# Kernel optimization log

Measured on AMD Instinct MI355X. Metric: run time of the kernel, lower is better.

## Reference

```python
import jax, jax.numpy as jnp
import numpy as np

# Module hyperparameters (from init_kwargs)
INPUT_SIZE = 1024
OUTPUT_SIZE = 1024
ORDER = 3
GRID_RANGE = (-1.0, 1.0)
GRID_COUNT = 8
CENTER_COUNT = GRID_COUNT + ORDER + 1  # 12

_lo, _hi = GRID_RANGE
_end_center = _hi + (_hi - _lo) * (ORDER + 1) / (GRID_COUNT - 1)
CENTERS = jnp.asarray(np.linspace(_lo, _end_center, CENTER_COUNT), dtype=jnp.float32)
ZOOM = (_hi - _lo) / 2.0
PAN = (_hi + _lo) / 2.0


def setup_inputs() -> dict:
    key = jax.random.key(0)
    k1, k2 = jax.random.split(key)
    x = jax.random.normal(k1, (4096, INPUT_SIZE), dtype=jnp.float32)
    coef = jax.random.normal(k2, (OUTPUT_SIZE, INPUT_SIZE, GRID_COUNT), dtype=jnp.float32) * 0.1
    return {"x": x, "coef": coef}


def _spline_basis(x):
    # x: [B, I] -> basis: [B, I, GRID_COUNT] via Cox-de Boor recursion
    xt = jnp.tanh(x) * ZOOM + PAN
    c = CENTERS
    xe = xt[..., None]  # [B, I, 1]
    # order-0: indicator of [c[i], c[i+1]) for i = 0..CENTER_COUNT-2
    b = ((xe >= c[:-1]) & (xe < c[1:])).astype(xt.dtype)  # [B, I, CENTER_COUNT-1]
    for k in range(1, ORDER + 1):
        n = CENTER_COUNT - k - 1
        c0, ck = c[:n], c[k:k + n]
        c1, ck1 = c[1:n + 1], c[k + 1:k + 1 + n]
        left = (xe - c0) / (ck - c0)          # [B, I, n]
        right = (ck1 - xe) / (ck1 - c1)       # [B, I, n]
        b = left * b[..., :n] + right * b[..., 1:n + 1]
    return b  # [B, I, GRID_COUNT]


def reference(x, coef):
    spline = _spline_basis(x)                      # [B, I, G]
    # sum_j over inputs of coef-weighted basis: [B, O]
    return jnp.einsum('big,oig->bo', spline, coef)
```

## Files before the change

kernel.cpp:

```cpp
#include <hip/hip_runtime.h>
#include <stdint.h>
#include <stddef.h>


#define BATCH 4096
#define IN    1024
#define OUTN  1024
#define KDIM  (IN * 8)
#define NTT   (KDIM / 64)

typedef __attribute__((ext_vector_type(8)))  short          short8;
typedef __attribute__((ext_vector_type(8)))  unsigned short ushort8;
typedef __attribute__((ext_vector_type(4)))  float          f32x4;


__device__ __forceinline__ constexpr float Cf(int i) {
    constexpr double end  = 1.0 + 2.0 * 4.0 / 7.0;
    constexpr double step = (end - (-1.0)) / 11.0;
    return (float)(-1.0 + (double)i * step);
}

__device__ __forceinline__ unsigned short f2bf(float f) {
    unsigned int u = __builtin_bit_cast(unsigned int, f);
    u += 0x7fffu + ((u >> 16) & 1u);
    return (unsigned short)(u >> 16);
}

__device__ __forceinline__ float bf2f(unsigned short u) {
    unsigned int v = (unsigned int)u << 16;
    return __builtin_bit_cast(float, v);
}

__device__ __forceinline__ ushort8 spline8(float xt) {
    float v[11];
#pragma unroll
    for (int j = 0; j < 11; ++j)
        v[j] = (xt >= Cf(j) && xt < Cf(j + 1)) ? 1.0f : 0.0f;
#pragma unroll
    for (int k = 1; k <= 3; ++k) {
#pragma unroll
        for (int j = 0; j < 11 - k; ++j) {
            float left  = (xt - Cf(j))         * (1.0f / (Cf(j + k)     - Cf(j)));
            float right = (Cf(j + k + 1) - xt) * (1.0f / (Cf(j + k + 1) - Cf(j + 1)));
            v[j] = left * v[j] + right * v[j + 1];
        }
    }
    ushort8 r;
#pragma unroll
    for (int g = 0; g < 8; ++g) r[g] = f2bf(v[g]);
    return r;
}

typedef const unsigned int __attribute__((address_space(1))) gu32;
typedef unsigned int       __attribute__((address_space(3))) lu32;

__device__ __forceinline__ void gload_lds16(const void* g, void* l) {
    __builtin_amdgcn_global_load_lds((gu32*)g, (lu32*)l, 16, 0, 0);
}


__global__ void prep_kernel(const float* __restrict__ x, const float* __restrict__ coef,
                            unsigned short* __restrict__ A, unsigned short* __restrict__ B) {
    const int t = threadIdx.x;
    int blk = blockIdx.x;
    if (blk < 4096) {
        const int bb = blk >> 4, bi = blk & 15;
        const int b  = bb * 16 + (t & 15);
        const int i0 = bi * 64 + (t >> 4) * 4;
        f32x4 xv = *reinterpret_cast<const f32x4*>(&x[(size_t)b * IN + i0]);
        ushort8 r[4];
#pragma unroll
        for (int j = 0; j < 4; ++j) r[j] = spline8(tanhf(xv[j]));
        ushort8* out = reinterpret_cast<ushort8*>(A)
                     + ((size_t)(bb * 256 + bi * 16 + (t >> 4)) * 64) + (t & 15);
        out[0]  = r[0];
        out[16] = r[1];
        out[32] = r[2];
        out[48] = r[3];
    } else {
        blk -= 4096;
        const int ob = blk >> 4, ib = blk & 15;
        const int oo = ob * 16 + (t & 15);
        const int i0 = ib * 64 + (t >> 4) * 4;
        const f32x4* cin = reinterpret_cast<const f32x4*>(coef);
        ushort8 r[4];
#pragma unroll
        for (int j = 0; j < 4; ++j) {
            f32x4 v0 = cin[((size_t)oo * IN + i0 + j) * 2];
            f32x4 v1 = cin[((size_t)oo * IN + i0 + j) * 2 + 1];
#pragma unroll
            for (int g = 0; g < 4; ++g) { r[j][g] = f2bf(v0[g]); r[j][4 + g] = f2bf(v1[g]); }
        }
        ushort8* out = reinterpret_cast<ushort8*>(B)
                     + ((size_t)(ob * 256 + ib * 16 + (t >> 4)) * 64) + (t & 15);
        out[0]  = r[0];
        out[16] = r[1];
        out[32] = r[2];
        out[48] = r[3];
    }
}


#define LSA0 (&Ls[0][0])
#define LSB0 (&Ls[0][16384])
#define LSA1 (&Ls[1][0])
#define LSB1 (&Ls[1][16384])

template<int NSPLIT>
__global__ __launch_bounds__(512, 2) void gemm_bt(
        const unsigned short* __restrict__ Ashuf,
        const unsigned short* __restrict__ Bshuf,
        float* __restrict__ C,
        unsigned short* __restrict__ P) {
    constexpr int NT2 = NTT / NSPLIT;
    static_assert((NT2 & 1) == 0, "loop assumes even NT2");
    __shared__ unsigned short Ls[2][32768];

    const int tid  = threadIdx.x;
    const int w    = tid >> 6;
    const int lane = tid & 63;
    const int wm   = w >> 2, wn = w & 3;
    const int kkw  = w & 1, wh = w >> 1;
    const int lane8 = lane * 8;

    const int bid  = blockIdx.x;
    const int s    = bid & (NSPLIT - 1);
    const int tile = bid / NSPLIT;
    const int mb16 = (tile >> 2) * 16;
    const int nb16 = (tile & 3) * 16;
    const int T0   = s * NT2;
    const int brow = mb16 * 16, bcol = nb16 * 16;

#define STAGE_OP(BASE, NB16, H, T, LS) do {                                   \
        size_t _kq = ((size_t)(2 * (T0 + (T)) + kkw)) * 512 + lane8;          \
        const unsigned short* _g = (BASE) + ((size_t)((NB16) + (H)*8 + wh) << 17) + _kq; \
        unsigned short* _l = (LS) + (((H)*16 + w) << 9);                      \
        gload_lds16(_g, _l);                                                  \
        gload_lds16(_g + ((size_t)4 << 17), _l + (8 << 9));                   \
    } while (0)
#define STAGE_A(H, T, LS) STAGE_OP(Ashuf, mb16, H, T, LS)
#define STAGE_B(H, T, LS) STAGE_OP(Bshuf, nb16, H, T, LS)

#define LDA_F(DST, H, LS) do {                                                \
        _Pragma("unroll")                                                     \
        for (int mf = 0; mf < 4; ++mf)                                        \
            _Pragma("unroll")                                                 \
            for (int kk = 0; kk < 2; ++kk)                                    \
                DST[mf][kk] = *reinterpret_cast<const short8*>(               \
                    (LS) + (((((H)*8 + wm*4 + mf) * 2) + kk) << 9) + lane8);  \
    } while (0)
#define LDB_F(DST, V, LS) do {                                                \
        _Pragma("unroll")                                                     \
        for (int nf = 0; nf < 2; ++nf)                                        \
            _Pragma("unroll")                                                 \
            for (int kk = 0; kk < 2; ++kk)                                    \
                DST[nf][kk] = *reinterpret_cast<const short8*>(               \
                    (LS) + (((((V)*8 + wn*2 + nf) * 2) + kk) << 9) + lane8);  \
    } while (0)

    f32x4 acc[8][4] = {};
    short8 aF[4][2], bv0[2][2], bv1[2][2];

#define MFMA_Q(H, V, AF, BV) do {                                             \
        __builtin_amdgcn_s_setprio(1);                                        \
        _Pragma("unroll")                                                     \
        for (int kk = 0; kk < 2; ++kk)                                        \
            _Pragma("unroll")                                                 \
            for (int mf = 0; mf < 4; ++mf)                                    \
                _Pragma("unroll")                                             \
                for (int nf = 0; nf < 2; ++nf)                                \
                    acc[(H)*4 + mf][(V)*2 + nf] =                             \
                        __builtin_amdgcn_mfma_f32_16x16x32_bf16(              \
                            AF[mf][kk], BV[nf][kk],                           \
                            acc[(H)*4 + mf][(V)*2 + nf], 0, 0, 0);            \
        __builtin_amdgcn_s_setprio(0);                                        \
    } while (0)

#define TILE(T, LAC, LBC, LAN, LBN, S1F, S23F, RN, VC) do {                   \
        __builtin_amdgcn_s_barrier();                                         \
        MFMA_Q(0, 0, aF, bv0);                                                \
        LDB_F(bv1, 1, LBC);                                                   \
        if (S1F) { STAGE_B(1, (T) + 1, LBN); STAGE_A(1, (T) + 1, LAN); }      \
        __builtin_amdgcn_s_barrier();                                         \
        MFMA_Q(0, 1, aF, bv1);                                                \
        LDA_F(aF, 1, LAC);                                                    \
        if (S23F) STAGE_B(0, (T) + 2, LBC);                                   \
        __builtin_amdgcn_s_barrier();                                         \
        MFMA_Q(1, 0, aF, bv0);                                                \
        if (S23F) STAGE_A(0, (T) + 2, LAC);                                   \
        asm volatile("s_waitcnt vmcnt(" VC ")" ::: "memory");                 \
        __builtin_amdgcn_s_barrier();                                         \
        MFMA_Q(1, 1, aF, bv1);                                                \
        if (RN) { LDA_F(aF, 0, LAN); LDB_F(bv0, 0, LBN); }                    \
    } while (0)

    STAGE_B(0, 0, LSB0); STAGE_A(0, 0, LSA0);
    STAGE_B(1, 0, LSB0); STAGE_A(1, 0, LSA0);
    STAGE_B(0, 1, LSB1); STAGE_A(0, 1, LSA1);
    asm volatile("s_waitcnt vmcnt(4)" ::: "memory");
    __builtin_amdgcn_s_barrier();
    LDA_F(aF, 0, LSA0); LDB_F(bv0, 0, LSB0);

#pragma unroll 1
    for (int t = 0; t + 2 <= NT2 - 2; t += 2) {
        TILE(t,     LSA0, LSB0, LSA1, LSB1, 1, 1, 1, "4");
        TILE(t + 1, LSA1, LSB1, LSA0, LSB0, 1, 1, 1, "4");
    }
    TILE(NT2 - 2, LSA0, LSB0, LSA1, LSB1, 1, 0, 1, "0");
    TILE(NT2 - 1, LSA1, LSB1, LSA0, LSB0, 0, 0, 0, "0");

    const int q4 = (lane >> 4) * 4, frow = lane & 15;
    if (NSPLIT == 1 || s == 0) {
#pragma unroll
        for (int H = 0; H < 2; ++H)
#pragma unroll
            for (int mf = 0; mf < 4; ++mf)
#pragma unroll
                for (int V = 0; V < 2; ++V)
#pragma unroll
                    for (int nf = 0; nf < 2; ++nf)
#pragma unroll
                        for (int r = 0; r < 4; ++r) {
                            int row = brow + H * 128 + wm * 64 + mf * 16 + q4 + r;
                            int col = bcol + V * 128 + wn * 32 + nf * 16 + frow;
                            C[(size_t)row * OUTN + col] = acc[H * 4 + mf][V * 2 + nf][r];
                        }
    } else {
        unsigned short* Pb = P + (size_t)(s - 1) * BATCH * OUTN;
#pragma unroll
        for (int H = 0; H < 2; ++H)
#pragma unroll
            for (int mf = 0; mf < 4; ++mf)
#pragma unroll
                for (int V = 0; V < 2; ++V)
#pragma unroll
                    for (int nf = 0; nf < 2; ++nf)
#pragma unroll
                        for (int r = 0; r < 4; ++r) {
                            int row = brow + H * 128 + wm * 64 + mf * 16 + q4 + r;
                            int col = bcol + V * 128 + wn * 32 + nf * 16 + frow;
                            Pb[(size_t)row * OUTN + col] = f2bf(acc[H * 4 + mf][V * 2 + nf][r]);
                        }
    }
}


__global__ void reduce_kernel(float* __restrict__ C, const unsigned short* __restrict__ P,
                              int np) {
    int i = blockIdx.x * 256 + threadIdx.x;
    size_t base = (size_t)i * 8;
    f32x4 c0 = *reinterpret_cast<f32x4*>(&C[base]);
    f32x4 c1 = *reinterpret_cast<f32x4*>(&C[base + 4]);
    for (int j = 0; j < np; ++j) {
        ushort8 p = *reinterpret_cast<const ushort8*>(&P[(size_t)j * BATCH * OUTN + base]);
#pragma unroll
        for (int e = 0; e < 4; ++e) c0[e] += bf2f(p[e]);
#pragma unroll
        for (int e = 0; e < 4; ++e) c1[e] += bf2f(p[4 + e]);
    }
    *reinterpret_cast<f32x4*>(&C[base])     = c0;
    *reinterpret_cast<f32x4*>(&C[base + 4]) = c1;
}


extern "C" void kernel_launch(void* const* d_in, const int* in_sizes, int n_in,
                              void* d_out, int out_size, void* d_ws, size_t ws_size,
                              hipStream_t stream) {
    const float* x    = (const float*)d_in[0];
    const float* coef = (const float*)d_in[1];
    float* out = (float*)d_out;

    unsigned short* ashuf = (unsigned short*)d_ws;
    unsigned short* bshuf = ashuf + (size_t)BATCH * KDIM;
    unsigned short* part  = bshuf + (size_t)OUTN * KDIM;
    const size_t base = (size_t)BATCH * KDIM * 2 + (size_t)OUTN * KDIM * 2;
    const size_t slab = (size_t)BATCH * OUTN * 2;

    prep_kernel<<<5120, 256, 0, stream>>>(x, coef, ashuf, bshuf);

    if (ws_size >= base + 3 * slab) {
        gemm_bt<4><<<256, 512, 0, stream>>>(ashuf, bshuf, out, part);
        reduce_kernel<<<2048, 256, 0, stream>>>(out, part, 3);
    } else if (ws_size >= base + slab) {
        gemm_bt<2><<<128, 512, 0, stream>>>(ashuf, bshuf, out, part);
        reduce_kernel<<<2048, 256, 0, stream>>>(out, part, 1);
    } else {
        gemm_bt<1><<<64, 512, 0, stream>>>(ashuf, bshuf, out, nullptr);
    }
}
```

Baseline: 96.43 us.

## Use 4 waves per block with 128x128 per-wave tiles in split-K GEMM

Moves the GEMM from 8 waves per 256x256 block (64x32 per wave) to 4 waves (128x128 per wave, 8x8 MFMA accumulators). Each wave now issues twice as many async global-to-LDS loads, and the vmcnt waits are raised to match. Larger per-wave tiles give more MFMA work per LDS fragment load, which cuts LDS read traffic. In exchange the 256 accumulator VGPRs per wave mean at most one block per CU, so less latency hiding and possible register pressure or spills.

```diff
diff --git a/kernel.cpp b/kernel.cpp
--- a/kernel.cpp
+++ b/kernel.cpp
@@ -107,20 +107,19 @@
 #define LSB1 (&Ls[1][16384])
 
 template<int NSPLIT>
-__global__ __launch_bounds__(512, 2) void gemm_bt(
+__global__ __launch_bounds__(256, 1) void gemm_bt(
         const unsigned short* __restrict__ Ashuf,
         const unsigned short* __restrict__ Bshuf,
         float* __restrict__ C,
         unsigned short* __restrict__ P) {
     constexpr int NT2 = NTT / NSPLIT;
-    static_assert((NT2 & 1) == 0, "loop assumes even NT2");
+    static_assert((NT2 & 1) == 0 && NT2 >= 8, "loop assumes even NT2 >= 8");
     __shared__ unsigned short Ls[2][32768];
 
     const int tid  = threadIdx.x;
     const int w    = tid >> 6;
     const int lane = tid & 63;
-    const int wm   = w >> 2, wn = w & 3;
-    const int kkw  = w & 1, wh = w >> 1;
+    const int wm   = w >> 1, wn = w & 1;
     const int lane8 = lane * 8;
 
     const int bid  = blockIdx.x;
@@ -132,79 +131,84 @@
     const int brow = mb16 * 16, bcol = nb16 * 16;
 
 #define STAGE_OP(BASE, NB16, H, T, LS) do {                                   \
-        size_t _kq = ((size_t)(2 * (T0 + (T)) + kkw)) * 512 + lane8;          \
-        const unsigned short* _g = (BASE) + ((size_t)((NB16) + (H)*8 + wh) << 17) + _kq; \
-        unsigned short* _l = (LS) + (((H)*16 + w) << 9);                      \
-        gload_lds16(_g, _l);                                                  \
-        gload_lds16(_g + ((size_t)4 << 17), _l + (8 << 9));                   \
+        _Pragma("unroll")                                                     \
+        for (int j = 0; j < 4; ++j) {                                         \
+            const int _rg = (H)*8 + w*2 + (j >> 1);                           \
+            const int _kk = j & 1;                                            \
+            const unsigned short* _g = (BASE)                                 \
+                + ((size_t)((NB16) + _rg) << 17)                              \
+                + ((size_t)(2 * (T0 + (T)) + _kk)) * 512 + lane8;             \
+            unsigned short* _l = (LS) + ((_rg * 2 + _kk) << 9);               \
+            gload_lds16(_g, _l);                                              \
+        }                                                                     \
     } while (0)
 #define STAGE_A(H, T, LS) STAGE_OP(Ashuf, mb16, H, T, LS)
 #define STAGE_B(H, T, LS) STAGE_OP(Bshuf, nb16, H, T, LS)
 
 #define LDA_F(DST, H, LS) do {                                                \
         _Pragma("unroll")                                                     \
-        for (int mf = 0; mf < 4; ++mf)                                        \
+        for (int i = 0; i < 4; ++i)                                           \
             _Pragma("unroll")                                                 \
             for (int kk = 0; kk < 2; ++kk)                                    \
-                DST[mf][kk] = *reinterpret_cast<const short8*>(               \
-                    (LS) + (((((H)*8 + wm*4 + mf) * 2) + kk) << 9) + lane8);  \
+                DST[i][kk] = *reinterpret_cast<const short8*>(                \
+                    (LS) + (((wm*8 + (H)*4 + i) * 2 + kk) << 9) + lane8);     \
     } while (0)
 #define LDB_F(DST, V, LS) do {                                                \
         _Pragma("unroll")                                                     \
-        for (int nf = 0; nf < 2; ++nf)                                        \
+        for (int j = 0; j < 4; ++j)                                           \
             _Pragma("unroll")                                                 \
             for (int kk = 0; kk < 2; ++kk)                                    \
-                DST[nf][kk] = *reinterpret_cast<const short8*>(               \
-                    (LS) + (((((V)*8 + wn*2 + nf) * 2) + kk) << 9) + lane8);  \
-    } while (0)
-
-    f32x4 acc[8][4] = {};
-    short8 aF[4][2], bv0[2][2], bv1[2][2];
-
-#define MFMA_Q(H, V, AF, BV) do {                                             \
+                DST[j][kk] = *reinterpret_cast<const short8*>(                \
+                    (LS) + (((wn*8 + (V)*4 + j) * 2 + kk) << 9) + lane8);     \
+    } while (0)
+
+    f32x4 acc[8][8] = {};
+    short8 aF[4][2], bv0[4][2], bv1[4][2];
+
+#define MFMA_Q(H, V, BV) do {                                                 \
         __builtin_amdgcn_s_setprio(1);                                        \
         _Pragma("unroll")                                                     \
         for (int kk = 0; kk < 2; ++kk)                                        \
             _Pragma("unroll")                                                 \
-            for (int mf = 0; mf < 4; ++mf)                                    \
+            for (int i = 0; i < 4; ++i)                                       \
                 _Pragma("unroll")                                             \
-                for (int nf = 0; nf < 2; ++nf)                                \
-                    acc[(H)*4 + mf][(V)*2 + nf] =                             \
+                for (int j = 0; j < 4; ++j)                                   \
+                    acc[(H)*4 + i][(V)*4 + j] =                               \
                         __builtin_amdgcn_mfma_f32_16x16x32_bf16(              \
-                            AF[mf][kk], BV[nf][kk],                           \
-                            acc[(H)*4 + mf][(V)*2 + nf], 0, 0, 0);            \
+                            aF[i][kk], BV[j][kk],                             \
+                            acc[(H)*4 + i][(V)*4 + j], 0, 0, 0);              \
         __builtin_amdgcn_s_setprio(0);                                        \
     } while (0)
 
 #define TILE(T, LAC, LBC, LAN, LBN, S1F, S23F, RN, VC) do {                   \
         __builtin_amdgcn_s_barrier();                                         \
-        MFMA_Q(0, 0, aF, bv0);                                                \
+        MFMA_Q(0, 0, bv0);                                                    \
         LDB_F(bv1, 1, LBC);                                                   \
         if (S1F) { STAGE_B(1, (T) + 1, LBN); STAGE_A(1, (T) + 1, LAN); }      \
         __builtin_amdgcn_s_barrier();                                         \
-        MFMA_Q(0, 1, aF, bv1);                                                \
+        MFMA_Q(0, 1, bv1);                                                    \
         LDA_F(aF, 1, LAC);                                                    \
         if (S23F) STAGE_B(0, (T) + 2, LBC);                                   \
         __builtin_amdgcn_s_barrier();                                         \
-        MFMA_Q(1, 0, aF, bv0);                                                \
+        MFMA_Q(1, 0, bv0);                                                    \
         if (S23F) STAGE_A(0, (T) + 2, LAC);                                   \
         asm volatile("s_waitcnt vmcnt(" VC ")" ::: "memory");                 \
         __builtin_amdgcn_s_barrier();                                         \
-        MFMA_Q(1, 1, aF, bv1);                                                \
+        MFMA_Q(1, 1, bv1);                                                    \
         if (RN) { LDA_F(aF, 0, LAN); LDB_F(bv0, 0, LBN); }                    \
     } while (0)
 
     STAGE_B(0, 0, LSB0); STAGE_A(0, 0, LSA0);
     STAGE_B(1, 0, LSB0); STAGE_A(1, 0, LSA0);
     STAGE_B(0, 1, LSB1); STAGE_A(0, 1, LSA1);
-    asm volatile("s_waitcnt vmcnt(4)" ::: "memory");
+    asm volatile("s_waitcnt vmcnt(8)" ::: "memory");
     __builtin_amdgcn_s_barrier();
     LDA_F(aF, 0, LSA0); LDB_F(bv0, 0, LSB0);
 
 #pragma unroll 1
     for (int t = 0; t + 2 <= NT2 - 2; t += 2) {
-        TILE(t,     LSA0, LSB0, LSA1, LSB1, 1, 1, 1, "4");
-        TILE(t + 1, LSA1, LSB1, LSA0, LSB0, 1, 1, 1, "4");
+        TILE(t,     LSA0, LSB0, LSA1, LSB1, 1, 1, 1, "8");
+        TILE(t + 1, LSA1, LSB1, LSA0, LSB0, 1, 1, 1, "8");
     }
     TILE(NT2 - 2, LSA0, LSB0, LSA1, LSB1, 1, 0, 1, "0");
     TILE(NT2 - 1, LSA1, LSB1, LSA0, LSB0, 0, 0, 0, "0");
@@ -212,35 +216,27 @@
     const int q4 = (lane >> 4) * 4, frow = lane & 15;
     if (NSPLIT == 1 || s == 0) {
 #pragma unroll
-        for (int H = 0; H < 2; ++H)
-#pragma unroll
-            for (int mf = 0; mf < 4; ++mf)
-#pragma unroll
-                for (int V = 0; V < 2; ++V)
-#pragma unroll
-                    for (int nf = 0; nf < 2; ++nf)
-#pragma unroll
-                        for (int r = 0; r < 4; ++r) {
-                            int row = brow + H * 128 + wm * 64 + mf * 16 + q4 + r;
-                            int col = bcol + V * 128 + wn * 32 + nf * 16 + frow;
-                            C[(size_t)row * OUTN + col] = acc[H * 4 + mf][V * 2 + nf][r];
-                        }
+        for (int mf = 0; mf < 8; ++mf)
+#pragma unroll
+            for (int nf = 0; nf < 8; ++nf)
+#pragma unroll
+                for (int r = 0; r < 4; ++r) {
+                    int row = brow + wm * 128 + mf * 16 + q4 + r;
+                    int col = bcol + wn * 128 + nf * 16 + frow;
+                    C[(size_t)row * OUTN + col] = acc[mf][nf][r];
+                }
     } else {
         unsigned short* Pb = P + (size_t)(s - 1) * BATCH * OUTN;
 #pragma unroll
-        for (int H = 0; H < 2; ++H)
-#pragma unroll
-            for (int mf = 0; mf < 4; ++mf)
-#pragma unroll
-                for (int V = 0; V < 2; ++V)
-#pragma unroll
-                    for (int nf = 0; nf < 2; ++nf)
-#pragma unroll
-                        for (int r = 0; r < 4; ++r) {
-                            int row = brow + H * 128 + wm * 64 + mf * 16 + q4 + r;
-                            int col = bcol + V * 128 + wn * 32 + nf * 16 + frow;
-                            Pb[(size_t)row * OUTN + col] = f2bf(acc[H * 4 + mf][V * 2 + nf][r]);
-                        }
+        for (int mf = 0; mf < 8; ++mf)
+#pragma unroll
+            for (int nf = 0; nf < 8; ++nf)
+#pragma unroll
+                for (int r = 0; r < 4; ++r) {
+                    int row = brow + wm * 128 + mf * 16 + q4 + r;
+                    int col = bcol + wn * 128 + nf * 16 + frow;
+                    Pb[(size_t)row * OUTN + col] = f2bf(acc[mf][nf][r]);
+                }
     }
 }
 
@@ -279,12 +275,12 @@
     prep_kernel<<<5120, 256, 0, stream>>>(x, coef, ashuf, bshuf);
 
     if (ws_size >= base + 3 * slab) {
-        gemm_bt<4><<<256, 512, 0, stream>>>(ashuf, bshuf, out, part);
+        gemm_bt<4><<<256, 256, 0, stream>>>(ashuf, bshuf, out, part);
         reduce_kernel<<<2048, 256, 0, stream>>>(out, part, 3);
     } else if (ws_size >= base + slab) {
-        gemm_bt<2><<<128, 512, 0, stream>>>(ashuf, bshuf, out, part);
+        gemm_bt<2><<<128, 256, 0, stream>>>(ashuf, bshuf, out, part);
         reduce_kernel<<<2048, 256, 0, stream>>>(out, part, 1);
     } else {
-        gemm_bt<1><<<64, 512, 0, stream>>>(ashuf, bshuf, out, nullptr);
-    }
-}
+        gemm_bt<1><<<64, 256, 0, stream>>>(ashuf, bshuf, out, nullptr);
+    }
+}
```

New measurement: 121.3 us. +25.8%, slower.
